# Optimization experiments

Measured on AMD Instinct MI355X. Metric: run time of the kernel, lower is better.

## Reference

```python
import jax, jax.numpy as jnp
import numpy as np

V, H, O = 32, 256, 256  # input_dim, hidden_dim, output_dim
EPS = 1e-5


def _layer_norm(x, g, b):
    m = jnp.mean(x, axis=-1, keepdims=True)
    v = jnp.mean((x - m) ** 2, axis=-1, keepdims=True)
    return g * (x - m) * jax.lax.rsqrt(v + EPS) + b


def setup_inputs() -> dict:
    key = jax.random.key(0)
    ks = jax.random.split(key, 20)
    s = 0.05
    inp = {
        "x": jax.random.normal(ks[0], (16, 256, V), dtype=jnp.float32),
        # selection GRN (input_dim -> input_dim, identity skip)
        "sel_fc1_w": jax.random.normal(ks[1], (V, H), dtype=jnp.float32) * s,
        "sel_fc1_b": jnp.zeros((H,), jnp.float32),
        "sel_fc2_w": jax.random.normal(ks[2], (H, V), dtype=jnp.float32) * s,
        "sel_fc2_b": jnp.zeros((V,), jnp.float32),
        "sel_gate_w": jax.random.normal(ks[3], (V, 2 * V), dtype=jnp.float32) * s,
        "sel_gate_b": jnp.zeros((2 * V,), jnp.float32),
        "sel_ln_g": jnp.ones((V,), jnp.float32),
        "sel_ln_b": jnp.zeros((V,), jnp.float32),
        # per-variable GRNs, stacked over the V variables (each has in_dim=1)
        "var_fc1_w": jax.random.normal(ks[4], (V, H), dtype=jnp.float32) * s,
        "var_fc1_b": jnp.zeros((V, H), jnp.float32),
        "var_fc2_w": jax.random.normal(ks[5], (V, H, O), dtype=jnp.float32) * s,
        "var_fc2_b": jnp.zeros((V, O), jnp.float32),
        "var_gate_w": jax.random.normal(ks[6], (V, 2 * O), dtype=jnp.float32) * s,
        "var_gate_b": jnp.zeros((V, 2 * O), jnp.float32),
        "var_skip_w": jax.random.normal(ks[7], (V, O), dtype=jnp.float32) * s,
        "var_skip_b": jnp.zeros((V, O), jnp.float32),
        "var_ln_g": jnp.ones((V, O), jnp.float32),
        "var_ln_b": jnp.zeros((V, O), jnp.float32),
    }
    return inp


def _vsn_forward(x, sel_fc1_w, sel_fc1_b, sel_fc2_w, sel_fc2_b, sel_gate_w,
                 sel_gate_b, sel_ln_g, sel_ln_b, var_fc1_w, var_fc1_b,
                 var_fc2_w, var_fc2_b, var_gate_w, var_gate_b, var_skip_w,
                 var_skip_b, var_ln_g, var_ln_b):
    B, S, _ = x.shape
    xr = x.reshape(-1, V)  # [N, V]

    # --- selection GRN (skip is identity) ---
    h = jax.nn.elu(xr @ sel_fc1_w + sel_fc1_b)        # [N, H]
    h = h @ sel_fc2_w + sel_fc2_b                      # [N, V] (unused by residual; matches torch code)
    g = xr @ sel_gate_w + sel_gate_b                   # [N, 2V]
    gates, values = jnp.split(g, 2, axis=-1)
    glu = jax.nn.sigmoid(gates) * values               # [N, V]
    sel = _layer_norm(glu + xr, sel_ln_g, sel_ln_b)    # [N, V]
    weights = jax.nn.softmax(sel, axis=-1)             # [N, V]

    # --- batched per-variable GRNs (in_dim = 1) ---
    xv = xr[..., None]                                  # [N, V, 1]
    hv = jax.nn.elu(xv * var_fc1_w + var_fc1_b)         # [N, V, H]
    hv = jnp.einsum('nvh,vho->nvo', hv, var_fc2_w) + var_fc2_b  # [N, V, O]
    gv = xv * var_gate_w + var_gate_b                   # [N, V, 2O]
    gates_v, values_v = jnp.split(gv, 2, axis=-1)
    glu_v = jax.nn.sigmoid(gates_v) * values_v          # [N, V, O]
    skip_v = xv * var_skip_w + var_skip_b               # [N, V, O]
    proc = _layer_norm(glu_v + skip_v, var_ln_g, var_ln_b)  # [N, V, O]

    out = jnp.einsum('nv,nvo->no', weights, proc)       # [N, O]
    return out.reshape(B, S, O)


def reference(x, sel_fc1_w, sel_fc1_b, sel_fc2_w, sel_fc2_b, sel_gate_w,
              sel_gate_b, sel_ln_g, sel_ln_b, var_fc1_w, var_fc1_b,
              var_fc2_w, var_fc2_b, var_gate_w, var_gate_b, var_skip_w,
              var_skip_b, var_ln_g, var_ln_b):
    return _vsn_forward(x, sel_fc1_w, sel_fc1_b, sel_fc2_w, sel_fc2_b,
                        sel_gate_w, sel_gate_b, sel_ln_g, sel_ln_b,
                        var_fc1_w, var_fc1_b, var_fc2_w, var_fc2_b,
                        var_gate_w, var_gate_b, var_skip_w, var_skip_b,
                        var_ln_g, var_ln_b)
```

## Files before the change

kernel.cpp:

```cpp
#include <hip/hip_runtime.h>
#include <hip/hip_bf16.h>


#define VDIM 32
#define ODIM 256
#define RPB  8
#define TPB  256
#define NCHUNK 16

__device__ __forceinline__ float fast_sigmoid(float g) {
    return __builtin_amdgcn_rcpf(1.0f + __expf(-g));
}

template <int CTRL>
__device__ __forceinline__ float dpp_add(float x) {
    int s = __builtin_amdgcn_update_dpp(0, __builtin_bit_cast(int, x),
                                        CTRL, 0xF, 0xF, true);
    return x + __builtin_bit_cast(float, s);
}

__device__ __forceinline__ float wave_sum(float x) {
    x = dpp_add<0x111>(x);
    x = dpp_add<0x112>(x);
    x = dpp_add<0x114>(x);
    x = dpp_add<0x118>(x);
    x = dpp_add<0x142>(x);
    x = dpp_add<0x143>(x);
    return __builtin_bit_cast(float,
        __builtin_amdgcn_readlane(__builtin_bit_cast(int, x), 63));
}

__global__ void __launch_bounds__(TPB) vsn_fused(
    const float* __restrict__ x,
    const float* __restrict__ sgw,
    const float* __restrict__ sgb,
    const float* __restrict__ slg,
    const float* __restrict__ slb,
    const float* __restrict__ vgw,
    const float* __restrict__ vgb,
    const float* __restrict__ vsw,
    const float* __restrict__ vsb,
    const float* __restrict__ vlg,
    const float* __restrict__ vlb,
    float* __restrict__ out)
{
    __shared__ float wbuf[2][4096];
    __shared__ float x_s[RPB][VDIM];
    __shared__ float g_s[RPB][2 * VDIM];
    __shared__ float w_s[RPB][VDIM];

    const int tid  = threadIdx.x;
    const int row0 = blockIdx.x * RPB;

    const float* p0 = vgw + (tid << 2);
    const float* p1 = vgb + (tid << 2);
    const float* p2 = (tid < 128 ? vsw : vsb - 512) + (tid << 2);
    const float* p3 = (tid < 128 ? vlg : vlb - 512) + (tid << 2);

    const float4 st0 = *(const float4*)p0;  p0 += 1024;
    const float4 st1 = *(const float4*)p1;  p1 += 1024;
    const float4 st2 = *(const float4*)p2;  p2 += 512;
    const float4 st3 = *(const float4*)p3;  p3 += 512;

    ((float*)x_s)[tid] = x[row0 * VDIM + tid];
    __syncthreads();

    #pragma unroll
    for (int it = 0; it < 2; ++it) {
        const int i = tid + it * TPB;
        const int r = i >> 6, j = i & 63;
        float acc = sgb[j];
        #pragma unroll
        for (int v = 0; v < VDIM; ++v)
            acc = fmaf(x_s[r][v], sgw[v * 64 + j], acc);
        g_s[r][j] = acc;
    }
    __syncthreads();

    {
        float4* wb = (float4*)wbuf[0];
        wb[tid]       = st0;
        wb[tid + 256] = st1;
        wb[tid + 512] = st2;
        wb[tid + 768] = st3;
    }

    {
        const int r = tid >> 5, v = tid & 31;
        const float gate = g_s[r][v];
        const float val  = g_s[r][VDIM + v];
        const float y    = fast_sigmoid(gate) * val + x_s[r][v];
        float s1 = y, s2 = y * y;
        #pragma unroll
        for (int m = 1; m < 32; m <<= 1) {
            s1 += __shfl_xor(s1, m, 64);
            s2 += __shfl_xor(s2, m, 64);
        }
        const float mean = s1 * (1.0f / VDIM);
        const float var  = s2 * (1.0f / VDIM) - mean * mean;
        const float rs   = __builtin_amdgcn_rsqf(var + 1e-5f);
        const float sel  = slg[v] * ((y - mean) * rs) + slb[v];
        float mx = sel;
        #pragma unroll
        for (int m = 1; m < 32; m <<= 1)
            mx = fmaxf(mx, __shfl_xor(mx, m, 64));
        const float e = __expf(sel - mx);
        float se = e;
        #pragma unroll
        for (int m = 1; m < 32; m <<= 1)
            se += __shfl_xor(se, m, 64);
        w_s[r][v] = e * __builtin_amdgcn_rcpf(se);
    }
    __syncthreads();

    const int wave = tid >> 6;
    const int lane = tid & 63;
    const int o0   = lane << 2;
    const int rA   = wave * 2, rB = rA + 1;

    float aA0 = 0.f, aA1 = 0.f, aA2 = 0.f, aA3 = 0.f;
    float aB0 = 0.f, aB1 = 0.f, aB2 = 0.f, aB3 = 0.f;

    for (int c = 0; c < NCHUNK; ++c) {
        float4 q0, q1, q2, q3;
        if (c < NCHUNK - 1) {
            q0 = *(const float4*)p0;  p0 += 1024;
            q1 = *(const float4*)p1;  p1 += 1024;
            q2 = *(const float4*)p2;  p2 += 512;
            q3 = *(const float4*)p3;  p3 += 512;
        }

        const float* buf = wbuf[c & 1];

        #pragma unroll
        for (int v4 = 0; v4 < 2; ++v4) {
            const int v = c * 2 + v4;
            const float4 ga  = *(const float4*)(buf + v4 * 512 + o0);
            const float4 va  = *(const float4*)(buf + v4 * 512 + 256 + o0);
            const float4 gab = *(const float4*)(buf + 1024 + v4 * 512 + o0);
            const float4 vab = *(const float4*)(buf + 1024 + v4 * 512 + 256 + o0);
            const float4 sw4 = *(const float4*)(buf + 2048 + v4 * 256 + o0);
            const float4 sb4 = *(const float4*)(buf + 2560 + v4 * 256 + o0);
            const float4 lg4 = *(const float4*)(buf + 3072 + v4 * 256 + o0);
            const float4 lb4 = *(const float4*)(buf + 3584 + v4 * 256 + o0);

            const float xa = x_s[rA][v];
            const float xb = x_s[rB][v];

            const float yA0 = fast_sigmoid(fmaf(xa, ga.x, gab.x)) * fmaf(xa, va.x, vab.x) + fmaf(xa, sw4.x, sb4.x);
            const float yA1 = fast_sigmoid(fmaf(xa, ga.y, gab.y)) * fmaf(xa, va.y, vab.y) + fmaf(xa, sw4.y, sb4.y);
            const float yA2 = fast_sigmoid(fmaf(xa, ga.z, gab.z)) * fmaf(xa, va.z, vab.z) + fmaf(xa, sw4.z, sb4.z);
            const float yA3 = fast_sigmoid(fmaf(xa, ga.w, gab.w)) * fmaf(xa, va.w, vab.w) + fmaf(xa, sw4.w, sb4.w);
            const float yB0 = fast_sigmoid(fmaf(xb, ga.x, gab.x)) * fmaf(xb, va.x, vab.x) + fmaf(xb, sw4.x, sb4.x);
            const float yB1 = fast_sigmoid(fmaf(xb, ga.y, gab.y)) * fmaf(xb, va.y, vab.y) + fmaf(xb, sw4.y, sb4.y);
            const float yB2 = fast_sigmoid(fmaf(xb, ga.z, gab.z)) * fmaf(xb, va.z, vab.z) + fmaf(xb, sw4.z, sb4.z);
            const float yB3 = fast_sigmoid(fmaf(xb, ga.w, gab.w)) * fmaf(xb, va.w, vab.w) + fmaf(xb, sw4.w, sb4.w);

            const float s1a = wave_sum((yA0 + yA1) + (yA2 + yA3));
            const float s2a = wave_sum(fmaf(yA0, yA0, fmaf(yA1, yA1, fmaf(yA2, yA2, yA3 * yA3))));
            const float s1b = wave_sum((yB0 + yB1) + (yB2 + yB3));
            const float s2b = wave_sum(fmaf(yB0, yB0, fmaf(yB1, yB1, fmaf(yB2, yB2, yB3 * yB3))));

            const float mA  = s1a * (1.0f / ODIM);
            const float vA  = s2a * (1.0f / ODIM) - mA * mA;
            const float rsA = __builtin_amdgcn_rsqf(vA + 1e-5f);
            const float wA  = w_s[rA][v];
            const float wrsA = wA * rsA;
            aA0 = fmaf(lg4.x, (yA0 - mA) * wrsA, fmaf(wA, lb4.x, aA0));
            aA1 = fmaf(lg4.y, (yA1 - mA) * wrsA, fmaf(wA, lb4.y, aA1));
            aA2 = fmaf(lg4.z, (yA2 - mA) * wrsA, fmaf(wA, lb4.z, aA2));
            aA3 = fmaf(lg4.w, (yA3 - mA) * wrsA, fmaf(wA, lb4.w, aA3));

            const float mB  = s1b * (1.0f / ODIM);
            const float vB  = s2b * (1.0f / ODIM) - mB * mB;
            const float rsB = __builtin_amdgcn_rsqf(vB + 1e-5f);
            const float wB  = w_s[rB][v];
            const float wrsB = wB * rsB;
            aB0 = fmaf(lg4.x, (yB0 - mB) * wrsB, fmaf(wB, lb4.x, aB0));
            aB1 = fmaf(lg4.y, (yB1 - mB) * wrsB, fmaf(wB, lb4.y, aB1));
            aB2 = fmaf(lg4.z, (yB2 - mB) * wrsB, fmaf(wB, lb4.z, aB2));
            aB3 = fmaf(lg4.w, (yB3 - mB) * wrsB, fmaf(wB, lb4.w, aB3));
        }

        if (c < NCHUNK - 1) {
            float4* wb = (float4*)wbuf[(c + 1) & 1];
            wb[tid]       = q0;
            wb[tid + 256] = q1;
            wb[tid + 512] = q2;
            wb[tid + 768] = q3;
        }
        __syncthreads();
    }

    *(float4*)(out + (size_t)(row0 + rA) * ODIM + o0) = make_float4(aA0, aA1, aA2, aA3);
    *(float4*)(out + (size_t)(row0 + rB) * ODIM + o0) = make_float4(aB0, aB1, aB2, aB3);
}

extern "C" void kernel_launch(void* const* d_in, const int* in_sizes, int n_in,
                              void* d_out, int out_size, void* d_ws, size_t ws_size,
                              hipStream_t stream) {
    const float* x   = (const float*)d_in[0];
    const float* sgw = (const float*)d_in[5];
    const float* sgb = (const float*)d_in[6];
    const float* slg = (const float*)d_in[7];
    const float* slb = (const float*)d_in[8];
    const float* vgw = (const float*)d_in[13];
    const float* vgb = (const float*)d_in[14];
    const float* vsw = (const float*)d_in[15];
    const float* vsb = (const float*)d_in[16];
    const float* vlg = (const float*)d_in[17];
    const float* vlb = (const float*)d_in[18];
    float* out = (float*)d_out;

    const int N = in_sizes[0] / VDIM;
    const int grid = N / RPB;

    vsn_fused<<<grid, TPB, 0, stream>>>(x, sgw, sgb, slg, slb,
                                        vgw, vgb, vsw, vsb, vlg, vlb, out);
}
```

Before: 115.6 us.

## Stage all per-variable weights in LDS as bf16 once, double rows per block

Replaces the chunked, double-buffered fp32 weight streaming with a single up-front load of all per-variable weights into shared memory, converted to bf16 with the gate weights pre-scaled by -log2(e) so the sigmoid uses exp2 directly. The block grows to 512 threads covering 16 rows, which removes the per-chunk barriers and halves the LDS read bandwidth per weight. x and the softmax weights are packed into one float2 array. This costs bf16 rounding of the weights, a heavy prologue per block, and 128KB of LDS that likely limits occupancy to one block per CU.

```diff
diff --git a/kernel.cpp b/kernel.cpp
--- a/kernel.cpp
+++ b/kernel.cpp
@@ -4,13 +4,9 @@
 
 #define VDIM 32
 #define ODIM 256
-#define RPB  8
-#define TPB  256
-#define NCHUNK 16
-
-__device__ __forceinline__ float fast_sigmoid(float g) {
-    return __builtin_amdgcn_rcpf(1.0f + __expf(-g));
-}
+#define RPB  16
+#define TPB  512
+#define NL2E (-1.4426950408889634f)
 
 template <int CTRL>
 __device__ __forceinline__ float dpp_add(float x) {
@@ -29,6 +25,21 @@
     return __builtin_bit_cast(float,
         __builtin_amdgcn_readlane(__builtin_bit_cast(int, x), 63));
 }
+
+__device__ __forceinline__ float fast_sigmoid(float g) {
+    return __builtin_amdgcn_rcpf(1.0f + __expf(-g));
+}
+
+__device__ __forceinline__ unsigned bf16rne(float f) {
+    unsigned u = __builtin_bit_cast(unsigned, f);
+    return (u + 0x7FFFu + ((u >> 16) & 1u)) >> 16;
+}
+__device__ __forceinline__ unsigned pack2(float lo, float hi) {
+    return bf16rne(lo) | (bf16rne(hi) << 16);
+}
+
+#define BFLO(u) __builtin_bit_cast(float, (u) << 16)
+#define BFHI(u) __builtin_bit_cast(float, (u) & 0xFFFF0000u)
 
 __global__ void __launch_bounds__(TPB) vsn_fused(
     const float* __restrict__ x,
@@ -44,25 +55,42 @@
     const float* __restrict__ vlb,
     float* __restrict__ out)
 {
-    __shared__ float wbuf[2][4096];
-    __shared__ float x_s[RPB][VDIM];
-    __shared__ float g_s[RPB][2 * VDIM];
-    __shared__ float w_s[RPB][VDIM];
+    __shared__ unsigned short wlds[32 * 2048];
+    __shared__ float2 xw_s[RPB][VDIM];
+    __shared__ float  g_s[RPB][2 * VDIM];
 
     const int tid  = threadIdx.x;
     const int row0 = blockIdx.x * RPB;
 
-    const float* p0 = vgw + (tid << 2);
-    const float* p1 = vgb + (tid << 2);
-    const float* p2 = (tid < 128 ? vsw : vsb - 512) + (tid << 2);
-    const float* p3 = (tid < 128 ? vlg : vlb - 512) + (tid << 2);
-
-    const float4 st0 = *(const float4*)p0;  p0 += 1024;
-    const float4 st1 = *(const float4*)p1;  p1 += 1024;
-    const float4 st2 = *(const float4*)p2;  p2 += 512;
-    const float4 st3 = *(const float4*)p3;  p3 += 512;
-
-    ((float*)x_s)[tid] = x[row0 * VDIM + tid];
+    xw_s[tid >> 5][tid & 31].x = x[row0 * VDIM + tid];
+
+    {
+        const int r = tid >> 1, h = tid & 1;
+        const int v = r >> 3, a = r & 7;
+        const float* src;
+        if (a == 0)      src = vgw + v * 512;
+        else if (a == 1) src = vgw + v * 512 + 256;
+        else if (a == 2) src = vgb + v * 512;
+        else if (a == 3) src = vgb + v * 512 + 256;
+        else if (a == 4) src = vsw + v * 256;
+        else if (a == 5) src = vsb + v * 256;
+        else if (a == 6) src = vlg + v * 256;
+        else             src = vlb + v * 256;
+        src += h * 128;
+        const float scale = (a == 0 || a == 2) ? NL2E : 1.0f;
+        unsigned short* dst = wlds + v * 2048 + a * 256 + h * 128;
+        #pragma unroll 4
+        for (int i = 0; i < 16; ++i) {
+            const float4 f0 = *(const float4*)(src + i * 8);
+            const float4 f1 = *(const float4*)(src + i * 8 + 4);
+            uint4 p;
+            p.x = pack2(f0.x * scale, f0.y * scale);
+            p.y = pack2(f0.z * scale, f0.w * scale);
+            p.z = pack2(f1.x * scale, f1.y * scale);
+            p.w = pack2(f1.z * scale, f1.w * scale);
+            *(uint4*)(dst + i * 8) = p;
+        }
+    }
     __syncthreads();
 
     #pragma unroll
@@ -72,24 +100,16 @@
         float acc = sgb[j];
         #pragma unroll
         for (int v = 0; v < VDIM; ++v)
-            acc = fmaf(x_s[r][v], sgw[v * 64 + j], acc);
+            acc = fmaf(xw_s[r][v].x, sgw[v * 64 + j], acc);
         g_s[r][j] = acc;
     }
     __syncthreads();
-
-    {
-        float4* wb = (float4*)wbuf[0];
-        wb[tid]       = st0;
-        wb[tid + 256] = st1;
-        wb[tid + 512] = st2;
-        wb[tid + 768] = st3;
-    }
 
     {
         const int r = tid >> 5, v = tid & 31;
         const float gate = g_s[r][v];
         const float val  = g_s[r][VDIM + v];
-        const float y    = fast_sigmoid(gate) * val + x_s[r][v];
+        const float y    = fast_sigmoid(gate) * val + xw_s[r][v].x;
         float s1 = y, s2 = y * y;
         #pragma unroll
         for (int m = 1; m < 32; m <<= 1) {
@@ -109,7 +129,7 @@
         #pragma unroll
         for (int m = 1; m < 32; m <<= 1)
             se += __shfl_xor(se, m, 64);
-        w_s[r][v] = e * __builtin_amdgcn_rcpf(se);
+        xw_s[r][v].y = e * __builtin_amdgcn_rcpf(se);
     }
     __syncthreads();
 
@@ -121,75 +141,59 @@
     float aA0 = 0.f, aA1 = 0.f, aA2 = 0.f, aA3 = 0.f;
     float aB0 = 0.f, aB1 = 0.f, aB2 = 0.f, aB3 = 0.f;
 
-    for (int c = 0; c < NCHUNK; ++c) {
-        float4 q0, q1, q2, q3;
-        if (c < NCHUNK - 1) {
-            q0 = *(const float4*)p0;  p0 += 1024;
-            q1 = *(const float4*)p1;  p1 += 1024;
-            q2 = *(const float4*)p2;  p2 += 512;
-            q3 = *(const float4*)p3;  p3 += 512;
-        }
-
-        const float* buf = wbuf[c & 1];
-
-        #pragma unroll
-        for (int v4 = 0; v4 < 2; ++v4) {
-            const int v = c * 2 + v4;
-            const float4 ga  = *(const float4*)(buf + v4 * 512 + o0);
-            const float4 va  = *(const float4*)(buf + v4 * 512 + 256 + o0);
-            const float4 gab = *(const float4*)(buf + 1024 + v4 * 512 + o0);
-            const float4 vab = *(const float4*)(buf + 1024 + v4 * 512 + 256 + o0);
-            const float4 sw4 = *(const float4*)(buf + 2048 + v4 * 256 + o0);
-            const float4 sb4 = *(const float4*)(buf + 2560 + v4 * 256 + o0);
-            const float4 lg4 = *(const float4*)(buf + 3072 + v4 * 256 + o0);
-            const float4 lb4 = *(const float4*)(buf + 3584 + v4 * 256 + o0);
-
-            const float xa = x_s[rA][v];
-            const float xb = x_s[rB][v];
-
-            const float yA0 = fast_sigmoid(fmaf(xa, ga.x, gab.x)) * fmaf(xa, va.x, vab.x) + fmaf(xa, sw4.x, sb4.x);
-            const float yA1 = fast_sigmoid(fmaf(xa, ga.y, gab.y)) * fmaf(xa, va.y, vab.y) + fmaf(xa, sw4.y, sb4.y);
-            const float yA2 = fast_sigmoid(fmaf(xa, ga.z, gab.z)) * fmaf(xa, va.z, vab.z) + fmaf(xa, sw4.z, sb4.z);
-            const float yA3 = fast_sigmoid(fmaf(xa, ga.w, gab.w)) * fmaf(xa, va.w, vab.w) + fmaf(xa, sw4.w, sb4.w);
-            const float yB0 = fast_sigmoid(fmaf(xb, ga.x, gab.x)) * fmaf(xb, va.x, vab.x) + fmaf(xb, sw4.x, sb4.x);
-            const float yB1 = fast_sigmoid(fmaf(xb, ga.y, gab.y)) * fmaf(xb, va.y, vab.y) + fmaf(xb, sw4.y, sb4.y);
-            const float yB2 = fast_sigmoid(fmaf(xb, ga.z, gab.z)) * fmaf(xb, va.z, vab.z) + fmaf(xb, sw4.z, sb4.z);
-            const float yB3 = fast_sigmoid(fmaf(xb, ga.w, gab.w)) * fmaf(xb, va.w, vab.w) + fmaf(xb, sw4.w, sb4.w);
-
-            const float s1a = wave_sum((yA0 + yA1) + (yA2 + yA3));
-            const float s2a = wave_sum(fmaf(yA0, yA0, fmaf(yA1, yA1, fmaf(yA2, yA2, yA3 * yA3))));
-            const float s1b = wave_sum((yB0 + yB1) + (yB2 + yB3));
-            const float s2b = wave_sum(fmaf(yB0, yB0, fmaf(yB1, yB1, fmaf(yB2, yB2, yB3 * yB3))));
-
-            const float mA  = s1a * (1.0f / ODIM);
-            const float vA  = s2a * (1.0f / ODIM) - mA * mA;
-            const float rsA = __builtin_amdgcn_rsqf(vA + 1e-5f);
-            const float wA  = w_s[rA][v];
-            const float wrsA = wA * rsA;
-            aA0 = fmaf(lg4.x, (yA0 - mA) * wrsA, fmaf(wA, lb4.x, aA0));
-            aA1 = fmaf(lg4.y, (yA1 - mA) * wrsA, fmaf(wA, lb4.y, aA1));
-            aA2 = fmaf(lg4.z, (yA2 - mA) * wrsA, fmaf(wA, lb4.z, aA2));
-            aA3 = fmaf(lg4.w, (yA3 - mA) * wrsA, fmaf(wA, lb4.w, aA3));
-
-            const float mB  = s1b * (1.0f / ODIM);
-            const float vB  = s2b * (1.0f / ODIM) - mB * mB;
-            const float rsB = __builtin_amdgcn_rsqf(vB + 1e-5f);
-            const float wB  = w_s[rB][v];
-            const float wrsB = wB * rsB;
-            aB0 = fmaf(lg4.x, (yB0 - mB) * wrsB, fmaf(wB, lb4.x, aB0));
-            aB1 = fmaf(lg4.y, (yB1 - mB) * wrsB, fmaf(wB, lb4.y, aB1));
-            aB2 = fmaf(lg4.z, (yB2 - mB) * wrsB, fmaf(wB, lb4.z, aB2));
-            aB3 = fmaf(lg4.w, (yB3 - mB) * wrsB, fmaf(wB, lb4.w, aB3));
-        }
-
-        if (c < NCHUNK - 1) {
-            float4* wb = (float4*)wbuf[(c + 1) & 1];
-            wb[tid]       = q0;
-            wb[tid + 256] = q1;
-            wb[tid + 512] = q2;
-            wb[tid + 768] = q3;
-        }
-        __syncthreads();
+    #pragma unroll 2
+    for (int v = 0; v < VDIM; ++v) {
+        const unsigned short* wv = wlds + v * 2048 + o0;
+        const uint2 Ugw = *(const uint2*)(wv);
+        const uint2 Uvw = *(const uint2*)(wv + 256);
+        const uint2 Ugb = *(const uint2*)(wv + 512);
+        const uint2 Uvb = *(const uint2*)(wv + 768);
+        const uint2 Usw = *(const uint2*)(wv + 1024);
+        const uint2 Usb = *(const uint2*)(wv + 1280);
+        const uint2 Ulg = *(const uint2*)(wv + 1536);
+        const uint2 Ulb = *(const uint2*)(wv + 1792);
+        const float2 XA = xw_s[rA][v];
+        const float2 XB = xw_s[rB][v];
+        const float xa = XA.x, wa = XA.y, xb = XB.x, wb = XB.y;
+
+        const float gw0 = BFLO(Ugw.x), gw1 = BFHI(Ugw.x), gw2 = BFLO(Ugw.y), gw3 = BFHI(Ugw.y);
+        const float vw0 = BFLO(Uvw.x), vw1 = BFHI(Uvw.x), vw2 = BFLO(Uvw.y), vw3 = BFHI(Uvw.y);
+        const float gb0 = BFLO(Ugb.x), gb1 = BFHI(Ugb.x), gb2 = BFLO(Ugb.y), gb3 = BFHI(Ugb.y);
+        const float vb0 = BFLO(Uvb.x), vb1 = BFHI(Uvb.x), vb2 = BFLO(Uvb.y), vb3 = BFHI(Uvb.y);
+        const float sw0 = BFLO(Usw.x), sw1 = BFHI(Usw.x), sw2 = BFLO(Usw.y), sw3 = BFHI(Usw.y);
+        const float sb0 = BFLO(Usb.x), sb1 = BFHI(Usb.x), sb2 = BFLO(Usb.y), sb3 = BFHI(Usb.y);
+        const float lg0 = BFLO(Ulg.x), lg1 = BFHI(Ulg.x), lg2 = BFLO(Ulg.y), lg3 = BFHI(Ulg.y);
+        const float lb0 = BFLO(Ulb.x), lb1 = BFHI(Ulb.x), lb2 = BFLO(Ulb.y), lb3 = BFHI(Ulb.y);
+
+        #define YV(xr, k) fmaf(__builtin_amdgcn_rcpf(1.0f + \
+            __builtin_amdgcn_exp2f(fmaf(xr, gw##k, gb##k))), \
+            fmaf(xr, vw##k, vb##k), fmaf(xr, sw##k, sb##k))
+        const float yA0 = YV(xa, 0), yA1 = YV(xa, 1), yA2 = YV(xa, 2), yA3 = YV(xa, 3);
+        const float yB0 = YV(xb, 0), yB1 = YV(xb, 1), yB2 = YV(xb, 2), yB3 = YV(xb, 3);
+        #undef YV
+
+        const float s1a = wave_sum((yA0 + yA1) + (yA2 + yA3));
+        const float s2a = wave_sum(fmaf(yA0, yA0, fmaf(yA1, yA1, fmaf(yA2, yA2, yA3 * yA3))));
+        const float s1b = wave_sum((yB0 + yB1) + (yB2 + yB3));
+        const float s2b = wave_sum(fmaf(yB0, yB0, fmaf(yB1, yB1, fmaf(yB2, yB2, yB3 * yB3))));
+
+        const float mA  = s1a * (1.0f / ODIM);
+        const float vA  = s2a * (1.0f / ODIM) - mA * mA;
+        const float rsA = __builtin_amdgcn_rsqf(vA + 1e-5f);
+        const float wrsA = wa * rsA;
+        aA0 = fmaf(lg0, (yA0 - mA) * wrsA, fmaf(wa, lb0, aA0));
+        aA1 = fmaf(lg1, (yA1 - mA) * wrsA, fmaf(wa, lb1, aA1));
+        aA2 = fmaf(lg2, (yA2 - mA) * wrsA, fmaf(wa, lb2, aA2));
+        aA3 = fmaf(lg3, (yA3 - mA) * wrsA, fmaf(wa, lb3, aA3));
+
+        const float mB  = s1b * (1.0f / ODIM);
+        const float vB  = s2b * (1.0f / ODIM) - mB * mB;
+        const float rsB = __builtin_amdgcn_rsqf(vB + 1e-5f);
+        const float wrsB = wb * rsB;
+        aB0 = fmaf(lg0, (yB0 - mB) * wrsB, fmaf(wb, lb0, aB0));
+        aB1 = fmaf(lg1, (yB1 - mB) * wrsB, fmaf(wb, lb1, aB1));
+        aB2 = fmaf(lg2, (yB2 - mB) * wrsB, fmaf(wb, lb2, aB2));
+        aB3 = fmaf(lg3, (yB3 - mB) * wrsB, fmaf(wb, lb3, aB3));
     }
 
     *(float4*)(out + (size_t)(row0 + rA) * ODIM + o0) = make_float4(aA0, aA1, aA2, aA3);
```

Result: slower. 133.9 us (+15.9%).
